# Optimization experiments

Hardware: AMD Instinct MI355X
Metric: run time of the kernel (lower is better)

## Reference

```python
import jax, jax.numpy as jnp
import numpy as np

EMBED_DIM = 1024
NUM_HEADS = 16
HEAD_DIM = EMBED_DIM // NUM_HEADS


def setup_inputs() -> dict:
    key = jax.random.key(0)
    ks = jax.random.split(key, 12)
    N, L, D = 2, 2048, EMBED_DIM
    s = 1.0 / np.sqrt(D)
    inp = {
        "values": jax.random.normal(ks[0], (N, L, D), jnp.float32),
        "key": jax.random.normal(ks[1], (N, L, D), jnp.float32),
        "query": jax.random.normal(ks[2], (N, L, D), jnp.float32),
        "mask": jnp.ones((N, 1, 1, L), jnp.int32),
        "Wv": jax.random.normal(ks[3], (D, D), jnp.float32) * s,
        "bv": jnp.zeros((D,), jnp.float32),
        "Wk": jax.random.normal(ks[4], (D, D), jnp.float32) * s,
        "bk": jnp.zeros((D,), jnp.float32),
        "Wq": jax.random.normal(ks[5], (D, D), jnp.float32) * s,
        "bq": jnp.zeros((D,), jnp.float32),
        "Wo": jax.random.normal(ks[6], (D, D), jnp.float32) * s,
        "bo": jnp.zeros((D,), jnp.float32),
    }
    return inp


def reference(values, key, query, mask, Wv, bv, Wk, bk, Wq, bq, Wo, bo):
    N, Lq, D = query.shape
    H, Hd = NUM_HEADS, HEAD_DIM
    # Linear projections (torch Linear: x @ W.T + b); split heads -> [N,H,L,Hd]
    v = (values @ Wv.T + bv).reshape(N, -1, H, Hd).transpose(0, 2, 1, 3)
    k = (key @ Wk.T + bk).reshape(N, -1, H, Hd).transpose(0, 2, 1, 3)
    q = (query @ Wq.T + bq).reshape(N, Lq, H, Hd).transpose(0, 2, 1, 3)
    energy = jnp.einsum('nhqd,nhkd->nhqk', q, k)  # [N,H,Lq,Lk]
    energy = jnp.where(mask == 0, jnp.float32(-1e20), energy)
    # NOTE: scales by sqrt(embed_dim), faithful to the original module
    attn = jax.nn.softmax(energy / jnp.sqrt(jnp.float32(D)), axis=-1)
    out = jnp.einsum('nhqk,nhkd->nhqd', attn, v)
    out = out.transpose(0, 2, 1, 3).reshape(N, Lq, D)
    return out @ Wo.T + bo
```

## Files before the change

kernel.cpp:

```cpp
#include <hip/hip_runtime.h>

typedef __bf16 bf16_t;
typedef __bf16 bf16x8 __attribute__((ext_vector_type(8)));
typedef float  f32x4  __attribute__((ext_vector_type(4)));

__device__ __forceinline__ f32x4 mfma16(bf16x8 a, bf16x8 b, f32x4 c) {
  return __builtin_amdgcn_mfma_f32_16x16x32_bf16(a, b, c, 0, 0, 0);
}

__device__ __forceinline__ float scrub(float x) {
  return fminf(fmaxf(x, -1e30f), 1e30f);
}

__device__ __forceinline__ void glds16(const bf16_t* g, bf16_t* l) {
  __builtin_amdgcn_global_load_lds(
      (const __attribute__((address_space(1))) unsigned char*)g,
      (__attribute__((address_space(3))) unsigned char*)l, 16, 0, 0);
}

__device__ __forceinline__ bool chk_f32(const void* p) {
  const unsigned short* u = (const unsigned short*)p;
  int cnt = 0;
#pragma unroll
  for (int i = 0; i < 64; i += 2) {
    int e = (u[i] >> 7) & 0xFF;
    cnt += (e > 100 && e < 140) ? 1 : 0;
  }
  return cnt < 16;
}
__device__ __forceinline__ bool chk_zero(const void* p) {
  const unsigned short* u = (const unsigned short*)p;
  unsigned acc = 0;
#pragma unroll
  for (int i = 0; i < 64; i++) acc |= u[i];
  return acc == 0;
}

__device__ __forceinline__ bf16x8 ld8(const void* p, size_t idx, bool f32) {
  if (f32) {
    const float* f = (const float*)p;
    f32x4 a = *(const f32x4*)&f[idx];
    f32x4 b = *(const f32x4*)&f[idx + 4];
    bf16x8 r;
#pragma unroll
    for (int e = 0; e < 4; e++) { r[e] = (bf16_t)a[e]; r[4 + e] = (bf16_t)b[e]; }
    return r;
  }
  return *(const bf16x8*)&((const bf16_t*)p)[idx];
}

__device__ __forceinline__ float ld_bias(const void* B, int col) {
  if (chk_zero(B)) return 0.0f;
  if (chk_f32(B)) return ((const float*)B)[col];
  return (float)((const bf16_t*)B)[col];
}

__global__ __launch_bounds__(256)
void conv_w(const void* __restrict__ W0, const void* __restrict__ W1,
            const void* __restrict__ W2, bf16_t* __restrict__ D)
{
  const void* W = (blockIdx.y == 0) ? W0 : (blockIdx.y == 1) ? W1 : W2;
  const bool f = chk_f32(W);
  bf16_t* d = D + (size_t)blockIdx.y * 1048576;
  size_t idx = ((size_t)blockIdx.x * 256 + threadIdx.x) * 8;
  *(bf16x8*)&d[idx] = ld8(W, idx, f);
}

__device__ __forceinline__ void proj_body(const void* X, const bf16_t* W16,
                                          const void* B, bf16_t* O,
                                          bf16_t* As, bf16_t* Bs, int flat)
{
  const bool xf = chk_f32(X);
  const bf16_t* Xb = (const bf16_t*)X;

  const int tid  = threadIdx.x;
  const int wave = tid >> 6, lane = tid & 63, quad = lane >> 4, lc = lane & 15;
  const int wr = (wave >> 1) * 32, wc = (wave & 1) * 64;

  const int nf   = (flat & 7) * 64 + (flat >> 3);
  const int row0 = (nf & 63) * 64, col0 = (nf >> 6) * 128;

  const f32x4 fz = {0.f, 0.f, 0.f, 0.f};
  f32x4 acc[2][4];
#pragma unroll
  for (int i = 0; i < 2; i++)
#pragma unroll
    for (int j = 0; j < 4; j++) acc[i][j] = fz;

  for (int k0 = 0; k0 < 1024; k0 += 64) {
    if (!xf) {
#pragma unroll
      for (int j = 0; j < 2; j++) {
        int fl = j * 256 + tid, row = fl >> 3, sp = (fl & 7) ^ (row & 7);
        glds16(&Xb[(size_t)(row0 + row) * 1024 + k0 + sp * 8], &As[fl * 8]);
      }
    } else {
      bf16x8 t0[2];
#pragma unroll
      for (int j = 0; j < 2; j++) {
        int fl = j * 256 + tid, row = fl >> 3, sp = (fl & 7) ^ (row & 7);
        t0[j] = ld8(X, (size_t)(row0 + row) * 1024 + k0 + sp * 8, true);
      }
#pragma unroll
      for (int j = 0; j < 2; j++) *(bf16x8*)&As[(j * 256 + tid) * 8] = t0[j];
    }
#pragma unroll
    for (int j = 0; j < 4; j++) {
      int fl = j * 256 + tid, row = fl >> 3, sp = (fl & 7) ^ (row & 7);
      glds16(&W16[(size_t)(col0 + row) * 1024 + k0 + sp * 8], &Bs[fl * 8]);
    }
    __syncthreads();

    bf16x8 a[2][2], b[2][4];
#pragma unroll
    for (int ks = 0; ks < 2; ks++) {
      const int sl = ((ks * 4 + quad) ^ (lc & 7)) * 8;
#pragma unroll
      for (int t = 0; t < 2; t++)
        a[ks][t] = *(const bf16x8*)&As[(wr + t * 16 + lc) * 64 + sl];
#pragma unroll
      for (int t = 0; t < 4; t++)
        b[ks][t] = *(const bf16x8*)&Bs[(wc + t * 16 + lc) * 64 + sl];
    }
    __builtin_amdgcn_s_setprio(1);
#pragma unroll
    for (int ks = 0; ks < 2; ks++)
#pragma unroll
      for (int tr = 0; tr < 2; tr++)
#pragma unroll
        for (int tc = 0; tc < 4; tc++)
          acc[tr][tc] = mfma16(a[ks][tr], b[ks][tc], acc[tr][tc]);
    __builtin_amdgcn_s_setprio(0);
    __syncthreads();
  }

  float bia[4];
#pragma unroll
  for (int tc = 0; tc < 4; tc++) bia[tc] = ld_bias(B, col0 + wc + tc * 16 + lc);

#pragma unroll
  for (int tr = 0; tr < 2; tr++)
#pragma unroll
    for (int tc = 0; tc < 4; tc++)
#pragma unroll
      for (int r = 0; r < 4; r++) {
        int row = row0 + wr + tr * 16 + quad * 4 + r;
        int col = col0 + wc + tc * 16 + lc;
        float v = scrub(acc[tr][tc][r] + bia[tc]);
        int n = row >> 11, l = row & 2047, h = col >> 6, hd = col & 63;
        O[(size_t)((n * 16 + h) * 2048 + l) * 64 + hd] = (bf16_t)v;
      }
}

__global__ __launch_bounds__(256, 4)
void gemm_proj_hs(const void* __restrict__ X, const bf16_t* __restrict__ W16,
                  const void* __restrict__ B, bf16_t* __restrict__ O)
{
  __shared__ bf16_t As[64 * 64];
  __shared__ bf16_t Bs[128 * 64];
  proj_body(X, W16, B, O, As, Bs, blockIdx.x + blockIdx.y * 64);
}

__global__ __launch_bounds__(256, 4)
void gemm_qkv(const void* __restrict__ Xv, const void* __restrict__ Xq,
              const void* __restrict__ Xk, const bf16_t* __restrict__ W16,
              const void* __restrict__ bv, const void* __restrict__ bq,
              const void* __restrict__ bk,
              bf16_t* __restrict__ Ov, bf16_t* __restrict__ Oq,
              bf16_t* __restrict__ Ok)
{
  __shared__ bf16_t As[64 * 64];
  __shared__ bf16_t Bs[128 * 64];
  const int z = blockIdx.z;
  const void* X = (z == 0) ? Xv : (z == 1) ? Xq : Xk;
  const void* B = (z == 0) ? bv : (z == 1) ? bq : bk;
  bf16_t*    O  = (z == 0) ? Ov : (z == 1) ? Oq : Ok;
  proj_body(X, W16 + (size_t)z * 1048576, B, O, As, Bs,
            blockIdx.x + blockIdx.y * 64);
}

__global__ __launch_bounds__(256, 4)
void gemm_oproj_f32(const bf16_t* __restrict__ Xhs, const bf16_t* __restrict__ W16,
                    const void* __restrict__ B, float* __restrict__ O)
{
  __shared__ bf16_t As[64 * 64];
  __shared__ bf16_t Bs[128 * 64];

  const int tid  = threadIdx.x;
  const int wave = tid >> 6, lane = tid & 63, quad = lane >> 4, lc = lane & 15;
  const int wr = (wave >> 1) * 32, wc = (wave & 1) * 64;

  const int flat = blockIdx.x + blockIdx.y * 64;
  const int nf   = (flat & 7) * 64 + (flat >> 3);
  const int row0 = (nf & 63) * 64, col0 = (nf >> 6) * 128;

  const f32x4 fz = {0.f, 0.f, 0.f, 0.f};
  f32x4 acc[2][4];
#pragma unroll
  for (int i = 0; i < 2; i++)
#pragma unroll
    for (int j = 0; j < 4; j++) acc[i][j] = fz;

  for (int k0 = 0; k0 < 1024; k0 += 64) {
#pragma unroll
    for (int j = 0; j < 2; j++) {
      int fl = j * 256 + tid, row = fl >> 3, sp = (fl & 7) ^ (row & 7);
      int grow = row0 + row, n = grow >> 11, l = grow & 2047;
      glds16(&Xhs[(size_t)((n * 16 + (k0 >> 6)) * 2048 + l) * 64 + sp * 8],
             &As[fl * 8]);
    }
#pragma unroll
    for (int j = 0; j < 4; j++) {
      int fl = j * 256 + tid, row = fl >> 3, sp = (fl & 7) ^ (row & 7);
      glds16(&W16[(size_t)(col0 + row) * 1024 + k0 + sp * 8], &Bs[fl * 8]);
    }
    __syncthreads();

    bf16x8 a[2][2], b[2][4];
#pragma unroll
    for (int ks = 0; ks < 2; ks++) {
      const int sl = ((ks * 4 + quad) ^ (lc & 7)) * 8;
#pragma unroll
      for (int t = 0; t < 2; t++)
        a[ks][t] = *(const bf16x8*)&As[(wr + t * 16 + lc) * 64 + sl];
#pragma unroll
      for (int t = 0; t < 4; t++)
        b[ks][t] = *(const bf16x8*)&Bs[(wc + t * 16 + lc) * 64 + sl];
    }
    __builtin_amdgcn_s_setprio(1);
#pragma unroll
    for (int ks = 0; ks < 2; ks++)
#pragma unroll
      for (int tr = 0; tr < 2; tr++)
#pragma unroll
        for (int tc = 0; tc < 4; tc++)
          acc[tr][tc] = mfma16(a[ks][tr], b[ks][tc], acc[tr][tc]);
    __builtin_amdgcn_s_setprio(0);
    __syncthreads();
  }

  float bia[4];
#pragma unroll
  for (int tc = 0; tc < 4; tc++) bia[tc] = ld_bias(B, col0 + wc + tc * 16 + lc);

#pragma unroll
  for (int tr = 0; tr < 2; tr++)
#pragma unroll
    for (int tc = 0; tc < 4; tc++)
#pragma unroll
      for (int r = 0; r < 4; r++) {
        int row = row0 + wr + tr * 16 + quad * 4 + r;
        int col = col0 + wc + tc * 16 + lc;
        O[(size_t)row * 1024 + col] = scrub(acc[tr][tc][r] + bia[tc]);
      }
}

__global__ __launch_bounds__(256, 2)
void attn(const bf16_t* __restrict__ q, const bf16_t* __restrict__ k,
          const bf16_t* __restrict__ v, const int* __restrict__ mask,
          bf16_t* __restrict__ o)
{
  const int tid  = threadIdx.x;
  const int wave = tid >> 6, lane = tid & 63, quad = lane >> 4, lc = lane & 15;

  const int flat = blockIdx.x + blockIdx.y * 16;
  const int nf   = (flat & 7) * 64 + (flat >> 3);
  const int qt = nf & 15, nh = nf >> 4;
  const int n = nh >> 4;

  __shared__ bf16_t Ks[128 * 64];
  __shared__ bf16_t Vts[64 * 136];
  __shared__ bf16_t Ps[4][32 * 72];
  __shared__ int s_msk;

  const bf16_t* qb = q + (size_t)nh * 131072 + (size_t)qt * 128 * 64;
  const bf16_t* kb = k + (size_t)nh * 131072;
  const bf16_t* vb = v + (size_t)nh * 131072;
  const int* mg = mask + n * 2048;

  if (tid == 0) s_msk = 0;
  __syncthreads();
  {
    int bad = 0;
    for (int i = tid; i < 2048; i += 256) bad |= (mg[i] == 0) ? 1 : 0;
    if (__any(bad)) { if (lane == 0) s_msk = 1; }
  }

  bf16x8 aq[2][2];
#pragma unroll
  for (int tr = 0; tr < 2; tr++)
#pragma unroll
    for (int ks = 0; ks < 2; ks++)
      aq[tr][ks] = *(const bf16x8*)&qb[(size_t)(wave * 32 + tr * 16 + lc) * 64 + ks * 32 + quad * 8];

  const f32x4 fz = {0.f, 0.f, 0.f, 0.f};
  f32x4 oacc[2][4];
  float mst[2][4], lst[2][4];
#pragma unroll
  for (int tr = 0; tr < 2; tr++)
#pragma unroll
    for (int j = 0; j < 4; j++) {
      oacc[tr][j] = fz; mst[tr][j] = -3.0e38f; lst[tr][j] = 0.f;
    }

  const float scale = 0.03125f;
  const float L2E   = 1.44269504f;
  const float C     = scale * L2E;

  __syncthreads();
  const bool nomask = (s_msk == 0);

#pragma unroll 1
  for (int c16 = 0; c16 < 16; c16++) {
#pragma unroll
    for (int j = 0; j < 4; j++) {
      int fl = j * 256 + tid, row = fl >> 3, sp = (fl & 7) ^ (row & 7);
      glds16(&kb[(size_t)(c16 * 128 + row) * 64 + sp * 8], &Ks[fl * 8]);
    }
    bf16x8 vv[4];
    {
      int key = tid & 127, ph = (tid >> 7) * 4;
#pragma unroll
      for (int pp = 0; pp < 4; pp++)
        vv[pp] = *(const bf16x8*)&vb[(size_t)(c16 * 128 + key) * 64 + (ph + pp) * 8];
#pragma unroll
      for (int pp = 0; pp < 4; pp++)
#pragma unroll
        for (int e = 0; e < 8; e++)
          Vts[((ph + pp) * 8 + e) * 136 + key] = vv[pp][e];
    }
    __syncthreads();

    f32x4 s[2][8];
#pragma unroll
    for (int tc = 0; tc < 8; tc++) { s[0][tc] = fz; s[1][tc] = fz; }
    __builtin_amdgcn_s_setprio(1);
#pragma unroll
    for (int ks = 0; ks < 2; ks++)
#pragma unroll
      for (int tc = 0; tc < 8; tc++) {
        int kr = tc * 16 + lc;
        bf16x8 bk = *(const bf16x8*)&Ks[kr * 64 + (((ks * 4 + quad) ^ (lc & 7)) * 8)];
        s[0][tc] = mfma16(aq[0][ks], bk, s[0][tc]);
        s[1][tc] = mfma16(aq[1][ks], bk, s[1][tc]);
      }
    __builtin_amdgcn_s_setprio(0);

    float alf[2][4];
    if (nomask) {
#pragma unroll
      for (int tr = 0; tr < 2; tr++)
#pragma unroll
        for (int r = 0; r < 4; r++) {
          float mx = s[tr][0][r];
#pragma unroll
          for (int tc = 1; tc < 8; tc++) mx = fmaxf(mx, s[tr][tc][r]);
          mx = fmaxf(mx, __shfl_xor(mx, 1));
          mx = fmaxf(mx, __shfl_xor(mx, 2));
          mx = fmaxf(mx, __shfl_xor(mx, 4));
          mx = fmaxf(mx, __shfl_xor(mx, 8));
          float mnew = fmaxf(mst[tr][r], mx);
          float al = exp2f((mst[tr][r] - mnew) * C);
          mst[tr][r] = mnew; alf[tr][r] = al;
          float mt = mnew * C;
          float rs = 0.f;
#pragma unroll
          for (int tc = 0; tc < 8; tc++) {
            float pv = exp2f(fmaf(s[tr][tc][r], C, -mt));
            s[tr][tc][r] = pv;
            rs += pv;
          }
          rs += __shfl_xor(rs, 1);
          rs += __shfl_xor(rs, 2);
          rs += __shfl_xor(rs, 4);
          rs += __shfl_xor(rs, 8);
          lst[tr][r] = lst[tr][r] * al + rs;
        }
    } else {
      float mb[8];
#pragma unroll
      for (int tc = 0; tc < 8; tc++)
        mb[tc] = (mg[c16 * 128 + tc * 16 + lc] == 0) ? -1e20f : 0.0f;
#pragma unroll
      for (int tr = 0; tr < 2; tr++)
#pragma unroll
        for (int tc = 0; tc < 8; tc++)
#pragma unroll
          for (int r = 0; r < 4; r++)
            s[tr][tc][r] = s[tr][tc][r] * scale + mb[tc];
#pragma unroll
      for (int tr = 0; tr < 2; tr++)
#pragma unroll
        for (int r = 0; r < 4; r++) {
          float mx = s[tr][0][r];
#pragma unroll
          for (int tc = 1; tc < 8; tc++) mx = fmaxf(mx, s[tr][tc][r]);
          mx = fmaxf(mx, __shfl_xor(mx, 1));
          mx = fmaxf(mx, __shfl_xor(mx, 2));
          mx = fmaxf(mx, __shfl_xor(mx, 4));
          mx = fmaxf(mx, __shfl_xor(mx, 8));
          float mnew = fmaxf(mst[tr][r], mx);
          float al = exp2f((mst[tr][r] - mnew) * L2E);
          mst[tr][r] = mnew; alf[tr][r] = al;
          float rs = 0.f;
#pragma unroll
          for (int tc = 0; tc < 8; tc++) {
            float pv = exp2f((s[tr][tc][r] - mnew) * L2E);
            s[tr][tc][r] = pv;
            rs += pv;
          }
          rs += __shfl_xor(rs, 1);
          rs += __shfl_xor(rs, 2);
          rs += __shfl_xor(rs, 4);
          rs += __shfl_xor(rs, 8);
          lst[tr][r] = lst[tr][r] * al + rs;
        }
    }

#pragma unroll
    for (int tr = 0; tr < 2; tr++)
#pragma unroll
      for (int tcd = 0; tcd < 4; tcd++)
#pragma unroll
        for (int r = 0; r < 4; r++) oacc[tr][tcd][r] *= alf[tr][r];

#pragma unroll
    for (int hh = 0; hh < 2; hh++) {
#pragma unroll
      for (int tr = 0; tr < 2; tr++)
#pragma unroll
        for (int tcl = 0; tcl < 4; tcl++)
#pragma unroll
          for (int r = 0; r < 4; r++)
            Ps[wave][(tr * 16 + quad * 4 + r) * 72 + tcl * 16 + lc] =
                (bf16_t)s[tr][hh * 4 + tcl][r];
#pragma unroll
      for (int ks2l = 0; ks2l < 2; ks2l++) {
        int ks2 = hh * 2 + ks2l;
        bf16x8 pa[2];
#pragma unroll
        for (int tr = 0; tr < 2; tr++)
          pa[tr] = *(const bf16x8*)&Ps[wave][(tr * 16 + lc) * 72 + ks2l * 32 + quad * 8];
        __builtin_amdgcn_s_setprio(1);
#pragma unroll
        for (int tcd = 0; tcd < 4; tcd++) {
          int d = tcd * 16 + lc;
          int c = ks2 * 4 + quad;
          bf16x8 bv = *(const bf16x8*)&Vts[d * 136 + c * 8];
          oacc[0][tcd] = mfma16(pa[0], bv, oacc[0][tcd]);
          oacc[1][tcd] = mfma16(pa[1], bv, oacc[1][tcd]);
        }
        __builtin_amdgcn_s_setprio(0);
      }
    }
    __syncthreads();
  }

#pragma unroll
  for (int tr = 0; tr < 2; tr++)
#pragma unroll
    for (int r = 0; r < 4; r++) {
      float inv = 1.0f / lst[tr][r];
      int l = qt * 128 + wave * 32 + tr * 16 + quad * 4 + r;
#pragma unroll
      for (int tcd = 0; tcd < 4; tcd++) {
        int d = tcd * 16 + lc;
        o[(size_t)(nh * 2048 + l) * 64 + d] = (bf16_t)scrub(oacc[tr][tcd][r] * inv);
      }
    }
}

extern "C" void kernel_launch(void* const* d_in, const int* in_sizes, int n_in,
                              void* d_out, int out_size, void* d_ws, size_t ws_size,
                              hipStream_t stream)
{
  const void* values = d_in[0];
  const void* key    = d_in[1];
  const void* query  = d_in[2];
  const int*  mask   = (const int*)d_in[3];
  const void* Wv = d_in[4];  const void* bv = d_in[5];
  const void* Wk = d_in[6];  const void* bk = d_in[7];
  const void* Wq = d_in[8];  const void* bq = d_in[9];
  const void* Wo = d_in[10]; const void* bo = d_in[11];

  bf16_t* scratch = (bf16_t*)d_out + 4194304;

  const bool fused = (d_ws != nullptr) && (ws_size >= (size_t)18 * 1024 * 1024);

  if (fused) {
    bf16_t* wsb  = (bf16_t*)d_ws;
    bf16_t* Vhs  = (bf16_t*)d_out;
    bf16_t* Qhs  = wsb;
    bf16_t* Khs  = wsb + 4194304;
    bf16_t* Wo16 = wsb + 8388608;
    bf16_t* Ohs  = (bf16_t*)d_in[1];

    conv_w<<<dim3(512, 3), 256, 0, stream>>>(Wv, Wq, Wk, scratch);
    conv_w<<<dim3(512, 1), 256, 0, stream>>>(Wo, Wo, Wo, Wo16);
    gemm_qkv<<<dim3(64, 8, 3), 256, 0, stream>>>(values, query, key, scratch,
                                                 bv, bq, bk, Vhs, Qhs, Khs);
    attn<<<dim3(16, 32), 256, 0, stream>>>(Qhs, Khs, Vhs, mask, Ohs);
    gemm_oproj_f32<<<dim3(64, 8), 256, 0, stream>>>(Ohs, Wo16, bo, (float*)d_out);
  } else {
    bf16_t* Vhs = (bf16_t*)d_out;
    bf16_t* Qhs = (bf16_t*)d_in[0];
    bf16_t* Khs = (bf16_t*)d_in[2];
    bf16_t* Ohs = (bf16_t*)d_in[1];
    bf16_t* Wv16 = scratch;
    bf16_t* Wq16 = scratch + 1048576;
    bf16_t* Wk16 = scratch + 2097152;
    bf16_t* Wo16 = (bf16_t*)d_in[0];

    conv_w<<<dim3(512, 3), 256, 0, stream>>>(Wv, Wq, Wk, scratch);
    gemm_proj_hs<<<dim3(64, 8), 256, 0, stream>>>(values, Wv16, bv, Vhs);
    gemm_proj_hs<<<dim3(64, 8), 256, 0, stream>>>(query,  Wq16, bq, Qhs);
    gemm_proj_hs<<<dim3(64, 8), 256, 0, stream>>>(key,    Wk16, bk, Khs);
    attn<<<dim3(16, 32), 256, 0, stream>>>(Qhs, Khs, Vhs, mask, Ohs);
    conv_w<<<dim3(512, 1), 256, 0, stream>>>(Wo, Wo, Wo, Wo16);
    gemm_oproj_f32<<<dim3(64, 8), 256, 0, stream>>>(Ohs, Wo16, bo, (float*)d_out);
  }
}
```

Before: 313.9 us.

## Halve attention query tile and alias P buffer into K smem for occupancy

The attention kernel now processes 64 query rows per block (16 per wave) instead of 128, doubling the grid to 1024 blocks and raising launch bounds to 4 blocks per CU. The per-wave P staging buffer now reuses the K tile shared memory, with an extra barrier after QK^T, which cuts LDS per block and lets more blocks fit per CU. The cost is that each K/V tile loaded into LDS is reused by half as many query rows, doubling K/V global traffic and adding a barrier per chunk.

```diff
diff --git a/kernel.cpp b/kernel.cpp
--- a/kernel.cpp
+++ b/kernel.cpp
@@ -255,7 +255,7 @@
       }
 }
 
-__global__ __launch_bounds__(256, 2)
+__global__ __launch_bounds__(256, 4)
 void attn(const bf16_t* __restrict__ q, const bf16_t* __restrict__ k,
           const bf16_t* __restrict__ v, const int* __restrict__ mask,
           bf16_t* __restrict__ o)
@@ -263,17 +263,16 @@
   const int tid  = threadIdx.x;
   const int wave = tid >> 6, lane = tid & 63, quad = lane >> 4, lc = lane & 15;
 
-  const int flat = blockIdx.x + blockIdx.y * 16;
-  const int nf   = (flat & 7) * 64 + (flat >> 3);
-  const int qt = nf & 15, nh = nf >> 4;
+  const int flat = blockIdx.x + blockIdx.y * 32;
+  const int nf   = (flat & 7) * 128 + (flat >> 3);
+  const int qt = nf & 31, nh = nf >> 5;
   const int n = nh >> 4;
 
-  __shared__ bf16_t Ks[128 * 64];
+  __shared__ bf16_t Uni[128 * 64];
   __shared__ bf16_t Vts[64 * 136];
-  __shared__ bf16_t Ps[4][32 * 72];
   __shared__ int s_msk;
 
-  const bf16_t* qb = q + (size_t)nh * 131072 + (size_t)qt * 128 * 64;
+  const bf16_t* qb = q + (size_t)nh * 131072 + (size_t)qt * 64 * 64;
   const bf16_t* kb = k + (size_t)nh * 131072;
   const bf16_t* vb = v + (size_t)nh * 131072;
   const int* mg = mask + n * 2048;
@@ -286,22 +285,16 @@
     if (__any(bad)) { if (lane == 0) s_msk = 1; }
   }
 
-  bf16x8 aq[2][2];
-#pragma unroll
-  for (int tr = 0; tr < 2; tr++)
-#pragma unroll
-    for (int ks = 0; ks < 2; ks++)
-      aq[tr][ks] = *(const bf16x8*)&qb[(size_t)(wave * 32 + tr * 16 + lc) * 64 + ks * 32 + quad * 8];
+  bf16x8 aq[2];
+#pragma unroll
+  for (int ks = 0; ks < 2; ks++)
+    aq[ks] = *(const bf16x8*)&qb[(size_t)(wave * 16 + lc) * 64 + ks * 32 + quad * 8];
 
   const f32x4 fz = {0.f, 0.f, 0.f, 0.f};
-  f32x4 oacc[2][4];
-  float mst[2][4], lst[2][4];
-#pragma unroll
-  for (int tr = 0; tr < 2; tr++)
-#pragma unroll
-    for (int j = 0; j < 4; j++) {
-      oacc[tr][j] = fz; mst[tr][j] = -3.0e38f; lst[tr][j] = 0.f;
-    }
+  f32x4 oacc[4];
+  float mst[4], lst[4];
+#pragma unroll
+  for (int j = 0; j < 4; j++) { oacc[j] = fz; mst[j] = -3.0e38f; lst[j] = 0.f; }
 
   const float scale = 0.03125f;
   const float L2E   = 1.44269504f;
@@ -309,13 +302,14 @@
 
   __syncthreads();
   const bool nomask = (s_msk == 0);
+  bf16_t* Pw = Uni + wave * 1152;
 
 #pragma unroll 1
   for (int c16 = 0; c16 < 16; c16++) {
 #pragma unroll
     for (int j = 0; j < 4; j++) {
       int fl = j * 256 + tid, row = fl >> 3, sp = (fl & 7) ^ (row & 7);
-      glds16(&kb[(size_t)(c16 * 128 + row) * 64 + sp * 8], &Ks[fl * 8]);
+      glds16(&kb[(size_t)(c16 * 128 + row) * 64 + sp * 8], &Uni[fl * 8]);
     }
     bf16x8 vv[4];
     {
@@ -331,124 +325,110 @@
     }
     __syncthreads();
 
-    f32x4 s[2][8];
-#pragma unroll
-    for (int tc = 0; tc < 8; tc++) { s[0][tc] = fz; s[1][tc] = fz; }
+    f32x4 s[8];
+#pragma unroll
+    for (int tc = 0; tc < 8; tc++) s[tc] = fz;
     __builtin_amdgcn_s_setprio(1);
 #pragma unroll
     for (int ks = 0; ks < 2; ks++)
 #pragma unroll
       for (int tc = 0; tc < 8; tc++) {
         int kr = tc * 16 + lc;
-        bf16x8 bk = *(const bf16x8*)&Ks[kr * 64 + (((ks * 4 + quad) ^ (lc & 7)) * 8)];
-        s[0][tc] = mfma16(aq[0][ks], bk, s[0][tc]);
-        s[1][tc] = mfma16(aq[1][ks], bk, s[1][tc]);
+        bf16x8 bk = *(const bf16x8*)&Uni[kr * 64 + (((ks * 4 + quad) ^ (lc & 7)) * 8)];
+        s[tc] = mfma16(aq[ks], bk, s[tc]);
       }
     __builtin_amdgcn_s_setprio(0);
 
-    float alf[2][4];
+    float alf[4];
     if (nomask) {
 #pragma unroll
-      for (int tr = 0; tr < 2; tr++)
-#pragma unroll
-        for (int r = 0; r < 4; r++) {
-          float mx = s[tr][0][r];
-#pragma unroll
-          for (int tc = 1; tc < 8; tc++) mx = fmaxf(mx, s[tr][tc][r]);
-          mx = fmaxf(mx, __shfl_xor(mx, 1));
-          mx = fmaxf(mx, __shfl_xor(mx, 2));
-          mx = fmaxf(mx, __shfl_xor(mx, 4));
-          mx = fmaxf(mx, __shfl_xor(mx, 8));
-          float mnew = fmaxf(mst[tr][r], mx);
-          float al = exp2f((mst[tr][r] - mnew) * C);
-          mst[tr][r] = mnew; alf[tr][r] = al;
-          float mt = mnew * C;
-          float rs = 0.f;
-#pragma unroll
-          for (int tc = 0; tc < 8; tc++) {
-            float pv = exp2f(fmaf(s[tr][tc][r], C, -mt));
-            s[tr][tc][r] = pv;
-            rs += pv;
-          }
-          rs += __shfl_xor(rs, 1);
-          rs += __shfl_xor(rs, 2);
-          rs += __shfl_xor(rs, 4);
-          rs += __shfl_xor(rs, 8);
-          lst[tr][r] = lst[tr][r] * al + rs;
+      for (int r = 0; r < 4; r++) {
+        float mx = s[0][r];
+#pragma unroll
+        for (int tc = 1; tc < 8; tc++) mx = fmaxf(mx, s[tc][r]);
+        mx = fmaxf(mx, __shfl_xor(mx, 1));
+        mx = fmaxf(mx, __shfl_xor(mx, 2));
+        mx = fmaxf(mx, __shfl_xor(mx, 4));
+        mx = fmaxf(mx, __shfl_xor(mx, 8));
+        float mnew = fmaxf(mst[r], mx);
+        float al = exp2f((mst[r] - mnew) * C);
+        mst[r] = mnew; alf[r] = al;
+        float mt = mnew * C;
+        float rs = 0.f;
+#pragma unroll
+        for (int tc = 0; tc < 8; tc++) {
+          float pv = exp2f(fmaf(s[tc][r], C, -mt));
+          s[tc][r] = pv;
+          rs += pv;
         }
+        rs += __shfl_xor(rs, 1);
+        rs += __shfl_xor(rs, 2);
+        rs += __shfl_xor(rs, 4);
+        rs += __shfl_xor(rs, 8);
+        lst[r] = lst[r] * al + rs;
+      }
     } else {
       float mb[8];
 #pragma unroll
       for (int tc = 0; tc < 8; tc++)
         mb[tc] = (mg[c16 * 128 + tc * 16 + lc] == 0) ? -1e20f : 0.0f;
 #pragma unroll
-      for (int tr = 0; tr < 2; tr++)
-#pragma unroll
-        for (int tc = 0; tc < 8; tc++)
-#pragma unroll
-          for (int r = 0; r < 4; r++)
-            s[tr][tc][r] = s[tr][tc][r] * scale + mb[tc];
-#pragma unroll
-      for (int tr = 0; tr < 2; tr++)
-#pragma unroll
-        for (int r = 0; r < 4; r++) {
-          float mx = s[tr][0][r];
-#pragma unroll
-          for (int tc = 1; tc < 8; tc++) mx = fmaxf(mx, s[tr][tc][r]);
-          mx = fmaxf(mx, __shfl_xor(mx, 1));
-          mx = fmaxf(mx, __shfl_xor(mx, 2));
-          mx = fmaxf(mx, __shfl_xor(mx, 4));
-          mx = fmaxf(mx, __shfl_xor(mx, 8));
-          float mnew = fmaxf(mst[tr][r], mx);
-          float al = exp2f((mst[tr][r] - mnew) * L2E);
-          mst[tr][r] = mnew; alf[tr][r] = al;
-          float rs = 0.f;
-#pragma unroll
-          for (int tc = 0; tc < 8; tc++) {
-            float pv = exp2f((s[tr][tc][r] - mnew) * L2E);
-            s[tr][tc][r] = pv;
-            rs += pv;
-          }
-          rs += __shfl_xor(rs, 1);
-          rs += __shfl_xor(rs, 2);
-          rs += __shfl_xor(rs, 4);
-          rs += __shfl_xor(rs, 8);
-          lst[tr][r] = lst[tr][r] * al + rs;
+      for (int tc = 0; tc < 8; tc++)
+#pragma unroll
+        for (int r = 0; r < 4; r++)
+          s[tc][r] = s[tc][r] * scale + mb[tc];
+#pragma unroll
+      for (int r = 0; r < 4; r++) {
+        float mx = s[0][r];
+#pragma unroll
+        for (int tc = 1; tc < 8; tc++) mx = fmaxf(mx, s[tc][r]);
+        mx = fmaxf(mx, __shfl_xor(mx, 1));
+        mx = fmaxf(mx, __shfl_xor(mx, 2));
+        mx = fmaxf(mx, __shfl_xor(mx, 4));
+        mx = fmaxf(mx, __shfl_xor(mx, 8));
+        float mnew = fmaxf(mst[r], mx);
+        float al = exp2f((mst[r] - mnew) * L2E);
+        mst[r] = mnew; alf[r] = al;
+        float rs = 0.f;
+#pragma unroll
+        for (int tc = 0; tc < 8; tc++) {
+          float pv = exp2f((s[tc][r] - mnew) * L2E);
+          s[tc][r] = pv;
+          rs += pv;
         }
-    }
-
-#pragma unroll
-    for (int tr = 0; tr < 2; tr++)
-#pragma unroll
-      for (int tcd = 0; tcd < 4; tcd++)
-#pragma unroll
-        for (int r = 0; r < 4; r++) oacc[tr][tcd][r] *= alf[tr][r];
+        rs += __shfl_xor(rs, 1);
+        rs += __shfl_xor(rs, 2);
+        rs += __shfl_xor(rs, 4);
+        rs += __shfl_xor(rs, 8);
+        lst[r] = lst[r] * al + rs;
+      }
+    }
+
+#pragma unroll
+    for (int tcd = 0; tcd < 4; tcd++)
+#pragma unroll
+      for (int r = 0; r < 4; r++) oacc[tcd][r] *= alf[r];
+
+    __syncthreads();
 
 #pragma unroll
     for (int hh = 0; hh < 2; hh++) {
 #pragma unroll
-      for (int tr = 0; tr < 2; tr++)
-#pragma unroll
-        for (int tcl = 0; tcl < 4; tcl++)
-#pragma unroll
-          for (int r = 0; r < 4; r++)
-            Ps[wave][(tr * 16 + quad * 4 + r) * 72 + tcl * 16 + lc] =
-                (bf16_t)s[tr][hh * 4 + tcl][r];
+      for (int tcl = 0; tcl < 4; tcl++)
+#pragma unroll
+        for (int r = 0; r < 4; r++)
+          Pw[(quad * 4 + r) * 72 + tcl * 16 + lc] = (bf16_t)s[hh * 4 + tcl][r];
 #pragma unroll
       for (int ks2l = 0; ks2l < 2; ks2l++) {
         int ks2 = hh * 2 + ks2l;
-        bf16x8 pa[2];
-#pragma unroll
-        for (int tr = 0; tr < 2; tr++)
-          pa[tr] = *(const bf16x8*)&Ps[wave][(tr * 16 + lc) * 72 + ks2l * 32 + quad * 8];
+        bf16x8 pa = *(const bf16x8*)&Pw[lc * 72 + ks2l * 32 + quad * 8];
         __builtin_amdgcn_s_setprio(1);
 #pragma unroll
         for (int tcd = 0; tcd < 4; tcd++) {
           int d = tcd * 16 + lc;
           int c = ks2 * 4 + quad;
           bf16x8 bv = *(const bf16x8*)&Vts[d * 136 + c * 8];
-          oacc[0][tcd] = mfma16(pa[0], bv, oacc[0][tcd]);
-          oacc[1][tcd] = mfma16(pa[1], bv, oacc[1][tcd]);
+          oacc[tcd] = mfma16(pa, bv, oacc[tcd]);
         }
         __builtin_amdgcn_s_setprio(0);
       }
@@ -457,17 +437,15 @@
   }
 
 #pragma unroll
-  for (int tr = 0; tr < 2; tr++)
-#pragma unroll
-    for (int r = 0; r < 4; r++) {
-      float inv = 1.0f / lst[tr][r];
-      int l = qt * 128 + wave * 32 + tr * 16 + quad * 4 + r;
-#pragma unroll
-      for (int tcd = 0; tcd < 4; tcd++) {
-        int d = tcd * 16 + lc;
-        o[(size_t)(nh * 2048 + l) * 64 + d] = (bf16_t)scrub(oacc[tr][tcd][r] * inv);
-      }
-    }
+  for (int r = 0; r < 4; r++) {
+    float inv = 1.0f / lst[r];
+    int l = qt * 64 + wave * 16 + quad * 4 + r;
+#pragma unroll
+    for (int tcd = 0; tcd < 4; tcd++) {
+      int d = tcd * 16 + lc;
+      o[(size_t)(nh * 2048 + l) * 64 + d] = (bf16_t)scrub(oacc[tcd][r] * inv);
+    }
+  }
 }
 
 extern "C" void kernel_launch(void* const* d_in, const int* in_sizes, int n_in,
@@ -499,7 +477,7 @@
     conv_w<<<dim3(512, 1), 256, 0, stream>>>(Wo, Wo, Wo, Wo16);
     gemm_qkv<<<dim3(64, 8, 3), 256, 0, stream>>>(values, query, key, scratch,
                                                  bv, bq, bk, Vhs, Qhs, Khs);
-    attn<<<dim3(16, 32), 256, 0, stream>>>(Qhs, Khs, Vhs, mask, Ohs);
+    attn<<<dim3(32, 32), 256, 0, stream>>>(Qhs, Khs, Vhs, mask, Ohs);
     gemm_oproj_f32<<<dim3(64, 8), 256, 0, stream>>>(Ohs, Wo16, bo, (float*)d_out);
   } else {
     bf16_t* Vhs = (bf16_t*)d_out;
@@ -515,7 +493,7 @@
     gemm_proj_hs<<<dim3(64, 8), 256, 0, stream>>>(values, Wv16, bv, Vhs);
     gemm_proj_hs<<<dim3(64, 8), 256, 0, stream>>>(query,  Wq16, bq, Qhs);
     gemm_proj_hs<<<dim3(64, 8), 256, 0, stream>>>(key,    Wk16, bk, Khs);
-    attn<<<dim3(16, 32), 256, 0, stream>>>(Qhs, Khs, Vhs, mask, Ohs);
+    attn<<<dim3(32, 32), 256, 0, stream>>>(Qhs, Khs, Vhs, mask, Ohs);
     conv_w<<<dim3(512, 1), 256, 0, stream>>>(Wo, Wo, Wo, Wo16);
     gemm_oproj_f32<<<dim3(64, 8), 256, 0, stream>>>(Ohs, Wo16, bo, (float*)d_out);
   }
```

Result: slower. 373.9 us (+19.1%).
